# Kernel optimization log

Measured on AMD Instinct MI355X. Metric: run time of the kernel, lower is better.

## Reference

```python
import jax, jax.numpy as jnp
import numpy as np

EMBED_DIM = 1024
NUM_HEADS = 16
HEAD_DIM = EMBED_DIM // NUM_HEADS


def setup_inputs() -> dict:
    key = jax.random.key(0)
    k1, k2, k3, k4 = jax.random.split(key, 4)
    B, S, D = 2, 2048, EMBED_DIM
    x = jax.random.normal(k1, (B, S, D), dtype=jnp.float32)
    xpos = jax.random.randint(k2, (B, S), 0, 2048, dtype=jnp.int32)
    # torch nn.Linear weights: [out_features, in_features]; qkv_bias=False -> no qkv bias
    qkv_w = jax.random.normal(k3, (3 * D, D), dtype=jnp.float32) * (D ** -0.5)
    proj_w = jax.random.normal(k4, (D, D), dtype=jnp.float32) * (D ** -0.5)
    proj_b = jnp.zeros((D,), dtype=jnp.float32)
    return {"x": x, "xpos": xpos, "qkv_w": qkv_w, "proj_w": proj_w, "proj_b": proj_b}


def reference(x, xpos, qkv_w, proj_w, proj_b):
    # rope is None, dropout rates are 0, so xpos is unused and dropout is identity.
    B, S, D = x.shape
    H, hd = NUM_HEADS, D // NUM_HEADS
    scale = hd ** -0.5

    qkv = x @ qkv_w.T                                   # [B, S, 3D]
    qkv = qkv.reshape(B, S, 3, H, hd)
    qkv = jnp.transpose(qkv, (0, 3, 2, 1, 4))           # [B, H, 3, S, hd]
    q, k, v = qkv[:, :, 0], qkv[:, :, 1], qkv[:, :, 2]  # each [B, H, S, hd]

    scores = jnp.einsum("bhqd,bhkd->bhqk", q, k) * scale  # [B, H, S, S]
    probs = jax.nn.softmax(scores, axis=-1)
    out = jnp.einsum("bhqk,bhkd->bhqd", probs, v)         # [B, H, S, hd]

    out = jnp.transpose(out, (0, 2, 1, 3)).reshape(B, S, D)
    out = out @ proj_w.T + proj_b
    return out
```

## Files before the change

kernel.cpp:

```cpp
#include <hip/hip_runtime.h>


typedef __bf16 bf16_8 __attribute__((ext_vector_type(8)));
typedef __bf16 bf16_4 __attribute__((ext_vector_type(4)));
typedef __bf16 bf16_2 __attribute__((ext_vector_type(2)));
typedef float floatx4 __attribute__((ext_vector_type(4)));
typedef float floatx16 __attribute__((ext_vector_type(16)));
typedef unsigned uintx4 __attribute__((ext_vector_type(4)));

#define MFMA16 __builtin_amdgcn_mfma_f32_16x16x32_bf16
#define MFMA32 __builtin_amdgcn_mfma_f32_32x32x16_bf16
#define CSCALE 0.1803368801111204f
#define EXP2R  __builtin_amdgcn_exp2f

__device__ __forceinline__ void gld16(const __bf16* g, __bf16* l) {
    __builtin_amdgcn_global_load_lds(
        (const __attribute__((address_space(1))) void*)g,
        (__attribute__((address_space(3))) void*)l, 16, 0, 0);
}

__device__ __forceinline__ unsigned pk_bf16(float a, float b) {
    bf16_2 t;
    t[0] = (__bf16)a; t[1] = (__bf16)b;
    return __builtin_bit_cast(unsigned, t);
}

__device__ __forceinline__ void pl32swap(unsigned& a, unsigned& b) {
    __asm__ __volatile__("v_permlane32_swap_b32 %0, %1" : "+v"(a), "+v"(b));
}

__global__ __launch_bounds__(256) void cvt_all(
    const float* __restrict__ x, const float* __restrict__ w1,
    const float* __restrict__ w2,
    __bf16* __restrict__ xb, __bf16* __restrict__ w1b, __bf16* __restrict__ w2b)
{
    const int i = blockIdx.x * 256 + threadIdx.x;
    const float* src; __bf16* dst; int off;
    if (i < (1 << 20))                  { src = x;  dst = xb;  off = i; }
    else if (i < (1 << 20) + 786432)    { src = w1; dst = w1b; off = i - (1 << 20); }
    else                                { src = w2; dst = w2b; off = i - (1 << 20) - 786432; }
    float4 v = ((const float4*)src)[off];
    bf16_4 o;
    o[0] = (__bf16)v.x; o[1] = (__bf16)v.y; o[2] = (__bf16)v.z; o[3] = (__bf16)v.w;
    ((bf16_4*)dst)[off] = o;
}

__global__ __launch_bounds__(256) void qkv_gemm(
    const __bf16* __restrict__ X, const __bf16* __restrict__ W,
    __bf16* __restrict__ q_ws, __bf16* __restrict__ k_ws, __bf16* __restrict__ vt_ws)
{
    __shared__ __align__(16) __bf16 S[2][2][128 * 64];

    const int tid = threadIdx.x, lane = tid & 63, wv = tid >> 6;
    const int quad = lane >> 4, l15 = lane & 15;
    const int wm = (wv >> 1) * 64, wn = (wv & 1) * 64;
    const int m0 = blockIdx.y * 128, n0 = blockIdx.x * 128;
    const int c = n0 >> 10;

    const __bf16* Abase;
    const __bf16* Bbase;
    if (c == 2) { Abase = X + (size_t)m0 * 1024; Bbase = W + (size_t)n0 * 1024; }
    else        { Abase = W + (size_t)n0 * 1024; Bbase = X + (size_t)m0 * 1024; }

    const int srow = tid >> 3, skc = tid & 7;
    const int ssw  = (skc ^ (srow & 7)) * 8;

#define QKV_STAGE(buf, k0)                                                     \
    {                                                                          \
        _Pragma("unroll")                                                      \
        for (int itg = 0; itg < 4; ++itg) {                                    \
            const int cc = itg * 256 + tid;                                    \
            const int row = srow + itg * 32;                                   \
            gld16(Abase + row * 1024 + (k0) + ssw, &S[buf][0][cc * 8]);        \
            gld16(Bbase + row * 1024 + (k0) + ssw, &S[buf][1][cc * 8]);        \
        }                                                                      \
    }

    floatx4 acc[4][4] = {};
    QKV_STAGE(0, 0)
    __syncthreads();

#pragma unroll 1
    for (int kk = 0; kk < 16; ++kk) {
        const int cur = kk & 1;
        if (kk < 15) QKV_STAGE(cur ^ 1, (kk + 1) * 64)

        const __bf16* As = S[cur][0];
        const __bf16* Bs = S[cur][1];
#pragma unroll
        for (int ks = 0; ks < 2; ++ks) {
            bf16_8 af[4], bf[4];
#pragma unroll
            for (int mt = 0; mt < 4; ++mt) {
                int r = wm + mt * 16 + l15;
                af[mt] = *(const bf16_8*)&As[r * 64 + (((ks * 4 + quad) ^ (r & 7)) * 8)];
            }
#pragma unroll
            for (int nt = 0; nt < 4; ++nt) {
                int r = wn + nt * 16 + l15;
                bf[nt] = *(const bf16_8*)&Bs[r * 64 + (((ks * 4 + quad) ^ (r & 7)) * 8)];
            }
#pragma unroll
            for (int mt = 0; mt < 4; ++mt)
#pragma unroll
                for (int nt = 0; nt < 4; ++nt)
                    acc[mt][nt] = MFMA16(af[mt], bf[nt], acc[mt][nt], 0, 0, 0);
        }

        if (kk < 15) {
            __asm__ __volatile__("s_waitcnt vmcnt(0)" ::: "memory");
            __syncthreads();
        }
    }

    if (c == 2) {
#pragma unroll
        for (int mt = 0; mt < 4; ++mt) {
            const int mbase = m0 + wm + mt * 16 + quad * 4;
            const int b = mbase >> 11, key0 = mbase & 2047;
#pragma unroll
            for (int nt = 0; nt < 4; ++nt) {
                const int n = n0 + wn + nt * 16 + l15;
                const int h = (n >> 6) & 15, d = n & 63;
                const int dt = d >> 5, l31v = d & 31;
                bf16_4 pk;
#pragma unroll
                for (int r = 0; r < 4; ++r) pk[r] = (__bf16)acc[mt][nt][r];
                const size_t off =
                    (((size_t)(b * 16 + h) * 32 + (key0 >> 6)) * 2 + dt) * 2048
                    + ((key0 >> 4) & 3) * 512
                    + (((key0 >> 3) & 1) * 32 + l31v) * 8 + (key0 & 7);
                *(bf16_4*)&vt_ws[off] = pk;
            }
        }
    } else {
        const float scale = (c == 1) ? CSCALE : 1.0f;
#pragma unroll
        for (int mt = 0; mt < 4; ++mt) {
            const int nn = n0 + wm + mt * 16 + quad * 4;
            const int h = (nn >> 6) & 15, d0 = nn & 63;
#pragma unroll
            for (int nt = 0; nt < 4; ++nt) {
                const int token = m0 + wn + nt * 16 + l15;
                const int b = token >> 11, key = token & 2047;
                bf16_4 pk;
#pragma unroll
                for (int r = 0; r < 4; ++r) pk[r] = (__bf16)(acc[mt][nt][r] * scale);
                if (c == 0) {
                    *(bf16_4*)&q_ws[((size_t)(b * 16 + h) * 2048 + key) * 64 + d0] = pk;
                } else {
                    const size_t off =
                        (((size_t)(b * 16 + h) * 32 + (key >> 6)) * 2 + ((key >> 5) & 1)) * 2048
                        + (d0 >> 4) * 512
                        + (((d0 >> 3) & 1) * 32 + (key & 31)) * 8 + (d0 & 7);
                    *(bf16_4*)&k_ws[off] = pk;
                }
            }
        }
    }
#undef QKV_STAGE
}

__global__ __launch_bounds__(256) void attn_kernel(
    const __bf16* __restrict__ q_ws, const __bf16* __restrict__ k_ws,
    const __bf16* __restrict__ vt_ws, __bf16* __restrict__ attn_ws)
{
    const int tid = threadIdx.x, lane = tid & 63, w = tid >> 6;
    const int l31 = lane & 31, hi = lane >> 5;

    const int linear = blockIdx.x + (blockIdx.y << 4);
    const int bh = ((linear & 7) << 2) + ((linear >> 3) & 3);
    const int qt = linear >> 5;
    const int q0 = qt * 128;

    const __bf16* __restrict__ qp  = q_ws  + (size_t)bh * (2048 * 64);
    const __bf16* __restrict__ kb0 = k_ws  + (size_t)bh * 131072;
    const __bf16* __restrict__ kb1 = kb0 + 2048;
    const __bf16* __restrict__ vb0 = vt_ws + (size_t)bh * 131072;
    const __bf16* __restrict__ vb1 = vb0 + 2048;

    const int vo = lane * 8;

    bf16_8 qf[4];
    {
        const int qrow = q0 + w * 32 + l31;
#pragma unroll
        for (int s = 0; s < 4; ++s)
            qf[s] = *(const bf16_8*)&qp[qrow * 64 + s * 16 + hi * 8];
    }

    floatx16 oacc[2] = {};
    float lsp[4] = {};

    bf16_8 ka[8], kb[8], va[8];
#pragma unroll
    for (int u = 0; u < 8; ++u)
        ka[u] = *(const bf16_8*)&(u < 4 ? kb0 : kb1)[vo + (u & 3) * 512];

#define ATTN_TILE(KC, KN, KT)                                                  \
    {                                                                          \
        const int ko  = (KT) * 4096 + vo;                                      \
        const int kon = ko + 4096;                                             \
        _Pragma("unroll")                                                      \
        for (int u = 0; u < 8; ++u)        \
            va[u] = *(const bf16_8*)&(u < 4 ? vb0 : vb1)[ko + (u & 3) * 512];  \
        floatx16 sacc[2] = {};                                                 \
        __builtin_amdgcn_s_setprio(1);                                         \
        _Pragma("unroll")                                                      \
        for (int s = 0; s < 4; ++s) {                                          \
            sacc[0] = MFMA32(KC[s],     qf[s], sacc[0], 0, 0, 0);              \
            sacc[1] = MFMA32(KC[4 + s], qf[s], sacc[1], 0, 0, 0);              \
        }                                                                      \
        __builtin_amdgcn_s_setprio(0);                                         \
        _Pragma("unroll")                                                      \
        for (int u = 0; u < 8; ++u)                       \
            KN[u] = *(const bf16_8*)&(u < 4 ? kb0 : kb1)[kon + (u & 3) * 512]; \
        unsigned D[2][4][2];                                                   \
        _Pragma("unroll")                                                      \
        for (int t = 0; t < 2; ++t)                                            \
            _Pragma("unroll")                                                  \
            for (int j = 0; j < 4; ++j)                                        \
                _Pragma("unroll")                                              \
                for (int e = 0; e < 2; ++e) {                                  \
                    float pa = EXP2R(sacc[t][j * 4 + e * 2]);                  \
                    float pb = EXP2R(sacc[t][j * 4 + e * 2 + 1]);              \
                    lsp[t * 2 + e] += pa + pb;                                 \
                    D[t][j][e] = pk_bf16(pa, pb);                              \
                }                                                              \
        __builtin_amdgcn_s_setprio(1);                                         \
        _Pragma("unroll")                                                      \
        for (int s = 0; s < 4; ++s) {                                          \
            const int t = s >> 1, b2 = (s & 1) * 2;                            \
            unsigned x0 = D[t][b2][0], y0 = D[t][b2 + 1][0];                   \
            unsigned x1 = D[t][b2][1], y1 = D[t][b2 + 1][1];                   \
            pl32swap(x0, y0);                                                  \
            pl32swap(x1, y1);                                                  \
            uintx4 uu; uu[0] = x0; uu[1] = x1; uu[2] = y0; uu[3] = y1;         \
            const bf16_8 pf = __builtin_bit_cast(bf16_8, uu);                  \
            oacc[0] = MFMA32(va[s],     pf, oacc[0], 0, 0, 0);                 \
            oacc[1] = MFMA32(va[4 + s], pf, oacc[1], 0, 0, 0);                 \
        }                                                                      \
        __builtin_amdgcn_s_setprio(0);                                         \
    }

#pragma unroll 1
    for (int it = 0; it < 16; ++it) {
        ATTN_TILE(ka, kb, (it * 2))
        ATTN_TILE(kb, ka, (it * 2 + 1))
    }
#undef ATTN_TILE

    const int b = bh >> 4, h = bh & 15;
    const float lsum = (lsp[0] + lsp[1]) + (lsp[2] + lsp[3]);
    const float lpart = __shfl_xor(lsum, 32, 64);
    const float inv_l = 1.0f / (lsum + lpart);
    const int token = b * 2048 + q0 + w * 32 + l31;
#pragma unroll
    for (int dt = 0; dt < 2; ++dt)
#pragma unroll
        for (int g = 0; g < 4; ++g) {
            bf16_4 ok;
#pragma unroll
            for (int r = 0; r < 4; ++r)
                ok[r] = (__bf16)(oacc[dt][g * 4 + r] * inv_l);
            *(bf16_4*)&attn_ws[(size_t)token * 1024 + h * 64 + dt * 32 + g * 8 + hi * 4] = ok;
        }
}

__device__ __forceinline__ void proj_stage(
    const __bf16* __restrict__ A, const __bf16* __restrict__ Bp,
    int k0, __bf16* As, __bf16* Bs, int tid)
{
#pragma unroll
    for (int it = 0; it < 4; ++it) {
        int cc = it * 256 + tid;
        int row = cc >> 3, kc = cc & 7;
        gld16(A + row * 1024 + k0 + ((kc ^ (row & 7)) * 8), &As[cc * 8]);
    }
#pragma unroll
    for (int it = 0; it < 2; ++it) {
        int cc = it * 256 + tid;
        int row = cc >> 3, kc = cc & 7;
        gld16(Bp + row * 1024 + k0 + ((kc ^ (row & 7)) * 8), &Bs[cc * 8]);
    }
}

__global__ __launch_bounds__(256) void proj_gemm(
    const __bf16* __restrict__ Ain, const __bf16* __restrict__ W,
    const float* __restrict__ bias, float* __restrict__ out)
{
    __shared__ __align__(16) __bf16 As[2][128 * 64];
    __shared__ __align__(16) __bf16 Bs[2][64 * 64];
    floatx4 acc[4][2] = {};
    const int m0 = blockIdx.y * 128, n0 = blockIdx.x * 64;

    const int tid = threadIdx.x, lane = tid & 63, wv = tid >> 6;
    const int quad = lane >> 4, l15 = lane & 15;
    const int wm = (wv >> 1) * 64, wn = (wv & 1) * 32;

    const __bf16* A  = Ain + (size_t)m0 * 1024;
    const __bf16* Bp = W   + (size_t)n0 * 1024;

    proj_stage(A, Bp, 0, As[0], Bs[0], tid);
    __syncthreads();

#pragma unroll 2
    for (int kk = 0; kk < 16; ++kk) {
        const int cur = kk & 1;
        if (kk < 15)
            proj_stage(A, Bp, (kk + 1) * 64, As[cur ^ 1], Bs[cur ^ 1], tid);

        const __bf16* Ab = As[cur];
        const __bf16* Bb = Bs[cur];
#pragma unroll
        for (int ks = 0; ks < 2; ++ks) {
            bf16_8 af[4], bf[2];
#pragma unroll
            for (int mt = 0; mt < 4; ++mt) {
                int r = wm + mt * 16 + l15;
                af[mt] = *(const bf16_8*)&Ab[r * 64 + (((ks * 4 + quad) ^ (r & 7)) * 8)];
            }
#pragma unroll
            for (int nt = 0; nt < 2; ++nt) {
                int r = wn + nt * 16 + l15;
                bf[nt] = *(const bf16_8*)&Bb[r * 64 + (((ks * 4 + quad) ^ (r & 7)) * 8)];
            }
#pragma unroll
            for (int mt = 0; mt < 4; ++mt)
#pragma unroll
                for (int nt = 0; nt < 2; ++nt)
                    acc[mt][nt] = MFMA16(af[mt], bf[nt], acc[mt][nt], 0, 0, 0);
        }

        if (kk < 15) {
            __asm__ __volatile__("s_waitcnt vmcnt(0)" ::: "memory");
            __syncthreads();
        }
    }

    float bv[2];
#pragma unroll
    for (int nt = 0; nt < 2; ++nt) bv[nt] = bias[n0 + wn + nt * 16 + l15];

#pragma unroll
    for (int mt = 0; mt < 4; ++mt) {
        const int m = m0 + wm + mt * 16 + quad * 4;
#pragma unroll
        for (int nt = 0; nt < 2; ++nt) {
            const int n = n0 + wn + nt * 16 + l15;
#pragma unroll
            for (int r = 0; r < 4; ++r)
                out[(size_t)(m + r) * 1024 + n] = acc[mt][nt][r] + bv[nt];
        }
    }
}

extern "C" void kernel_launch(void* const* d_in, const int* in_sizes, int n_in,
                              void* d_out, int out_size, void* d_ws, size_t ws_size,
                              hipStream_t stream)
{
    const float* x      = (const float*)d_in[0];
    const float* qkv_w  = (const float*)d_in[2];
    const float* proj_w = (const float*)d_in[3];
    const float* proj_b = (const float*)d_in[4];
    float* out = (float*)d_out;

    const size_t SZ   = 4096 * 1024;
    const size_t WQKV = 3072 * 1024;
    const size_t WPRJ = 1024 * 1024;

    __bf16* xb      = (__bf16*)d_ws;
    __bf16* qkvwb   = xb + SZ;
    __bf16* projwb  = qkvwb + WQKV;
    __bf16* q_ws    = projwb + WPRJ;
    __bf16* k_ws    = q_ws + SZ;
    __bf16* vt_ws   = k_ws + SZ;
    __bf16* attn_ws = vt_ws + SZ;

    cvt_all<<<dim3(8192), 256, 0, stream>>>(x, qkv_w, proj_w, xb, qkvwb, projwb);
    qkv_gemm  <<<dim3(24, 32), 256, 0, stream>>>(xb, qkvwb, q_ws, k_ws, vt_ws);
    attn_kernel<<<dim3(16, 32), 256, 0, stream>>>(q_ws, k_ws, vt_ws, attn_ws);
    proj_gemm <<<dim3(16, 32), 256, 0, stream>>>(attn_ws, projwb, proj_b, out);
}
```

Before: 178.0 us.

## Split attention key range across waves and combine partial outputs in LDS

Each attention block now handles 64 queries, with its four waves split into two query tiles and two key halves. Each wave processes half the keys. The second key half writes its partial accumulators and row sums to shared memory, and the first half adds them before normalizing and storing. The grid doubles to 1024 blocks to raise parallelism and balance load across CUs. The cost is an extra LDS round trip, a block barrier, and duplicated Q loads per key half.

```diff
diff --git a/kernel.cpp b/kernel.cpp
--- a/kernel.cpp
+++ b/kernel.cpp
@@ -165,25 +165,30 @@
     const __bf16* __restrict__ q_ws, const __bf16* __restrict__ k_ws,
     const __bf16* __restrict__ vt_ws, __bf16* __restrict__ attn_ws)
 {
+    __shared__ __align__(16) floatx4 comb[2][8][64];
+    __shared__ float lcomb[2][64];
+
     const int tid = threadIdx.x, lane = tid & 63, w = tid >> 6;
     const int l31 = lane & 31, hi = lane >> 5;
-
-    const int linear = blockIdx.x + (blockIdx.y << 4);
-    const int bh = ((linear & 7) << 2) + ((linear >> 3) & 3);
-    const int qt = linear >> 5;
-    const int q0 = qt * 128;
+    const int qtile = w & 1, keyhalf = w >> 1;
+
+    const int linear = blockIdx.x + (blockIdx.y << 5);
+    const int r = linear >> 3;
+    const int bh = ((linear & 7) << 2) + (r & 3);
+    const int qblk = r >> 2;
+    const int q0 = qblk * 64 + qtile * 32;
 
     const __bf16* __restrict__ qp  = q_ws  + (size_t)bh * (2048 * 64);
-    const __bf16* __restrict__ kb0 = k_ws  + (size_t)bh * 131072;
+    const __bf16* __restrict__ kb0 = k_ws  + (size_t)bh * 131072 + keyhalf * 65536;
     const __bf16* __restrict__ kb1 = kb0 + 2048;
-    const __bf16* __restrict__ vb0 = vt_ws + (size_t)bh * 131072;
+    const __bf16* __restrict__ vb0 = vt_ws + (size_t)bh * 131072 + keyhalf * 65536;
     const __bf16* __restrict__ vb1 = vb0 + 2048;
 
     const int vo = lane * 8;
 
     bf16_8 qf[4];
     {
-        const int qrow = q0 + w * 32 + l31;
+        const int qrow = q0 + l31;
 #pragma unroll
         for (int s = 0; s < 4; ++s)
             qf[s] = *(const bf16_8*)&qp[qrow * 64 + s * 16 + hi * 8];
@@ -244,27 +249,44 @@
     }
 
 #pragma unroll 1
-    for (int it = 0; it < 16; ++it) {
+    for (int it = 0; it < 8; ++it) {
         ATTN_TILE(ka, kb, (it * 2))
         ATTN_TILE(kb, ka, (it * 2 + 1))
     }
 #undef ATTN_TILE
 
-    const int b = bh >> 4, h = bh & 15;
     const float lsum = (lsp[0] + lsp[1]) + (lsp[2] + lsp[3]);
-    const float lpart = __shfl_xor(lsum, 32, 64);
-    const float inv_l = 1.0f / (lsum + lpart);
-    const int token = b * 2048 + q0 + w * 32 + l31;
-#pragma unroll
-    for (int dt = 0; dt < 2; ++dt)
-#pragma unroll
-        for (int g = 0; g < 4; ++g) {
-            bf16_4 ok;
-#pragma unroll
-            for (int r = 0; r < 4; ++r)
-                ok[r] = (__bf16)(oacc[dt][g * 4 + r] * inv_l);
-            *(bf16_4*)&attn_ws[(size_t)token * 1024 + h * 64 + dt * 32 + g * 8 + hi * 4] = ok;
-        }
+    const float lw = lsum + __shfl_xor(lsum, 32, 64);
+
+    if (keyhalf == 1) {
+#pragma unroll
+        for (int dt = 0; dt < 2; ++dt)
+#pragma unroll
+            for (int g = 0; g < 4; ++g) {
+                floatx4 v4;
+#pragma unroll
+                for (int r4 = 0; r4 < 4; ++r4) v4[r4] = oacc[dt][g * 4 + r4];
+                comb[qtile][dt * 4 + g][lane] = v4;
+            }
+        lcomb[qtile][lane] = lw;
+    }
+    __syncthreads();
+    if (keyhalf == 0) {
+        const int b = bh >> 4, h = bh & 15;
+        const float inv_l = 1.0f / (lw + lcomb[qtile][lane]);
+        const int token = b * 2048 + q0 + l31;
+#pragma unroll
+        for (int dt = 0; dt < 2; ++dt)
+#pragma unroll
+            for (int g = 0; g < 4; ++g) {
+                const floatx4 v2 = comb[qtile][dt * 4 + g][lane];
+                bf16_4 ok;
+#pragma unroll
+                for (int r4 = 0; r4 < 4; ++r4)
+                    ok[r4] = (__bf16)((oacc[dt][g * 4 + r4] + v2[r4]) * inv_l);
+                *(bf16_4*)&attn_ws[(size_t)token * 1024 + h * 64 + dt * 32 + g * 8 + hi * 4] = ok;
+            }
+    }
 }
 
 __device__ __forceinline__ void proj_stage(
@@ -379,6 +401,6 @@
 
     cvt_all<<<dim3(8192), 256, 0, stream>>>(x, qkv_w, proj_w, xb, qkvwb, projwb);
     qkv_gemm  <<<dim3(24, 32), 256, 0, stream>>>(xb, qkvwb, q_ws, k_ws, vt_ws);
-    attn_kernel<<<dim3(16, 32), 256, 0, stream>>>(q_ws, k_ws, vt_ws, attn_ws);
+    attn_kernel<<<dim3(32, 32), 256, 0, stream>>>(q_ws, k_ws, vt_ws, attn_ws);
     proj_gemm <<<dim3(16, 32), 256, 0, stream>>>(attn_ws, projwb, proj_b, out);
 }
```

Result: slower. 184.1 us (+3.4%).
